# Kernel tuning notes

Measured on AMD Instinct MI355X. Metric: run time of the kernel, lower is better.

## Reference

```python
import jax, jax.numpy as jnp
import numpy as np

B = 16384
D = 384
K = 256
BETAS = (0.05, 0.25, 0.6)  # per-level commitment costs


def setup_inputs() -> dict:
    key = jax.random.key(0)
    k0, k1, k2, kc0, kc1, kc2 = jax.random.split(key, 6)
    return {
        "l0": jax.random.normal(k0, (B, 4, D), dtype=jnp.float32),
        "l1": jax.random.normal(k1, (B, 16, D), dtype=jnp.float32),
        "l2": jax.random.normal(k2, (B, 16, D), dtype=jnp.float32),
        "cb0": jax.random.normal(kc0, (K, D), dtype=jnp.float32),
        "cb1": jax.random.normal(kc1, (K, D), dtype=jnp.float32),
        "cb2": jax.random.normal(kc2, (K, D), dtype=jnp.float32),
    }


def _vq(x, cb, beta):
    # x: (B, T, D), cb: (K, D) -> d2: (B, T, K)
    d2 = (jnp.sum(x * x, axis=-1, keepdims=True)
          - 2.0 * jnp.einsum('btd,kd->btk', x, cb)
          + jnp.sum(cb * cb, axis=-1))
    idx = jnp.argmin(d2, axis=-1)            # (B, T) nearest codebook entry
    q = cb[idx]                              # (B, T, D) gather
    # EMA-VQ: codebook updated by EMA, loss is commitment term only
    loss = beta * jnp.mean((jax.lax.stop_gradient(q) - x) ** 2)
    q_st = x + jax.lax.stop_gradient(q - x)  # straight-through estimator
    return q_st, loss, idx


def reference(l0, l1, l2, cb0, cb1, cb2):
    q0, loss0, idx0 = _vq(l0, cb0, BETAS[0])
    q1, loss1, idx1 = _vq(l1, cb1, BETAS[1])
    q2, loss2, idx2 = _vq(l2, cb2, BETAS[2])
    total_vq_loss = loss0 + loss1 + loss2
    return (q0, q1, q2, total_vq_loss, idx0, idx1, idx2)
```

## Files before the change

kernel.cpp:

```cpp
#include <hip/hip_runtime.h>

static constexpr int KN  = 256;
static constexpr int DD  = 384;
static constexpr int DD4 = 96;
static constexpr int TM  = 64;
#define FLAG_MARGIN 0.005f

typedef __attribute__((ext_vector_type(8)))  short bf16x8;
typedef __attribute__((ext_vector_type(16))) float f32x16;
typedef __attribute__((ext_vector_type(4)))  short short4v;

__device__ __forceinline__ unsigned short f2bf_rne(float x) {
  unsigned u = __float_as_uint(x);
  return (unsigned short)((u + 0x7fffu + ((u >> 16) & 1u)) >> 16);
}

__device__ __forceinline__ void g2lds16(const void* g, void* l) {
  __builtin_amdgcn_global_load_lds(
      (const __attribute__((address_space(1))) unsigned int*)g,
      (__attribute__((address_space(3))) unsigned int*)l, 16, 0, 0);
}

__device__ __forceinline__ float emu_sq_pairwise384(const float* __restrict__ p) {
  float S[4];
#pragma unroll
  for (int blk = 0; blk < 4; ++blk) {
    const float* b = p + blk * 96;
    float r[8];
#pragma unroll
    for (int l = 0; l < 8; ++l) r[l] = __fmul_rn(b[l], b[l]);
    for (int j = 8; j < 96; j += 8) {
#pragma unroll
      for (int l = 0; l < 8; ++l) r[l] = __fadd_rn(r[l], __fmul_rn(b[j + l], b[j + l]));
    }
    float t1 = __fadd_rn(__fadd_rn(r[0], r[1]), __fadd_rn(r[2], r[3]));
    float t2 = __fadd_rn(__fadd_rn(r[4], r[5]), __fadd_rn(r[6], r[7]));
    S[blk] = __fadd_rn(t1, t2);
  }
  return __fadd_rn(__fadd_rn(S[0], S[1]), __fadd_rn(S[2], S[3]));
}

__device__ __forceinline__ float emu_dot384_np(const float* __restrict__ x,
                                               const float* __restrict__ c) {
  float s[16];
#pragma unroll
  for (int t = 0; t < 16; ++t) s[t] = 0.f;
  for (int j = 0; j < 384; j += 16) {
#pragma unroll
    for (int t = 0; t < 16; ++t)
      s[t] = __fadd_rn(__fmul_rn(x[j + t], c[j + t]), s[t]);
  }
  float w0 = __fadd_rn(__fadd_rn(s[0], s[4]), __fadd_rn(s[8],  s[12]));
  float w1 = __fadd_rn(__fadd_rn(s[1], s[5]), __fadd_rn(s[9],  s[13]));
  float w2 = __fadd_rn(__fadd_rn(s[2], s[6]), __fadd_rn(s[10], s[14]));
  float w3 = __fadd_rn(__fadd_rn(s[3], s[7]), __fadd_rn(s[11], s[15]));
  return __fadd_rn(__fadd_rn(w0, w1), __fadd_rn(w2, w3));
}

__global__ __launch_bounds__(256) void prep_kernel(const float* __restrict__ c0,
                                                   const float* __restrict__ c1,
                                                   const float* __restrict__ c2,
                                                   float* __restrict__ e2,
                                                   double* __restrict__ delta,
                                                   short* __restrict__ fragbase) {
  int bid = blockIdx.x;
  if (bid < 3) {
    const float* cb = (bid == 0) ? c0 : ((bid == 1) ? c1 : c2);
    e2[bid * KN + threadIdx.x] = emu_sq_pairwise384(cb + (size_t)threadIdx.x * DD);
    if (threadIdx.x == 0) delta[bid] = 0.0;
    return;
  }
  int sb = bid - 3;
  int lvl = sb / 48;
  int blk48 = sb - lvl * 48;
  const float* cb = (lvl == 0) ? c0 : ((lvl == 1) ? c1 : c2);
  short* frag = fragbase + (size_t)lvl * 196608;
  int gid = blk48 * 256 + threadIdx.x;
  int e = gid / 48;
  int g = gid - e * 48;
  const float4* s4 = reinterpret_cast<const float4*>(cb) + (size_t)e * 96 + g * 2;
  float4 v0 = s4[0], v1 = s4[1];
  float xs[8] = {v0.x, v0.y, v0.z, v0.w, v1.x, v1.y, v1.z, v1.w};
  short h[8], l[8];
#pragma unroll
  for (int i = 0; i < 8; ++i) {
    h[i] = (short)f2bf_rne(xs[i]);
    float hf = __uint_as_float((unsigned)(unsigned short)h[i] << 16);
    l[i] = (short)f2bf_rne(xs[i] - hf);
  }
  int c = g >> 2, rem = g & 3, ks = rem >> 1, hs = rem & 1;
  int t = e >> 5, lane = (e & 31) + (hs << 5);
  size_t blk = (((size_t)(c * 8 + t) * 2 + ks) * 2);
  short* dh = frag + blk * 512 + lane * 8;
  short* dl = dh + 512;
  *reinterpret_cast<bf16x8*>(dh) = *reinterpret_cast<const bf16x8*>(h);
  *reinterpret_cast<bf16x8*>(dl) = *reinterpret_cast<const bf16x8*>(l);
}

__global__ __launch_bounds__(512) void vq_main(
    const float* __restrict__ X0, const float* __restrict__ X1, const float* __restrict__ X2,
    const float* __restrict__ C0, const float* __restrict__ C1, const float* __restrict__ C2,
    const short* __restrict__ FRAGBASE,
    const float* __restrict__ E2A,
    float* __restrict__ QBASE,
    float* __restrict__ IDXBASE,
    unsigned char* __restrict__ FLAGBASE,
    double* __restrict__ PART,
    int nb0, int nb1)
{
  __shared__ __align__(16) short cb_lds[16384];
  __shared__ __align__(16) short x_lds[4096];
  struct Epi {
    float b1[8][TM]; int i1[8][TM]; float b2[8][TM];
    int idx[TM]; float xx[TM];
  };
  Epi* ep = reinterpret_cast<Epi*>(x_lds);

  const int bid = blockIdx.x;
  int lvl, lb;
  if (bid < nb0)            { lvl = 0; lb = bid; }
  else if (bid < nb0 + nb1) { lvl = 1; lb = bid - nb0; }
  else                      { lvl = 2; lb = bid - nb0 - nb1; }
  const float* X  = (lvl == 0) ? X0 : ((lvl == 1) ? X1 : X2);
  const float* CBF32 = (lvl == 0) ? C0 : ((lvl == 1) ? C1 : C2);
  const short* CBFRAG = FRAGBASE + (size_t)lvl * 196608;
  const float* E2 = E2A + lvl * KN;
  const size_t rowbase = (lvl == 0) ? 0 : ((lvl == 1) ? (size_t)nb0 * TM
                                                      : (size_t)(nb0 + nb1) * TM);
  float* Q = QBASE + rowbase * DD;
  float* IDXO = IDXBASE + rowbase;
  unsigned char* FLAG = FLAGBASE + rowbase;
  const size_t row0 = (size_t)lb * TM;

  const int tid  = threadIdx.x;
  const int wid  = tid >> 6, lane = tid & 63;
  const int lr   = lane & 31, hi = lane >> 5;
  const int r_st = tid >> 3, k4 = tid & 7;

  const float4* X4 = reinterpret_cast<const float4*>(X);
  const float4* xsrc = X4 + (row0 + (size_t)r_st) * DD4 + k4;

  f32x16 acc[2];
  {
    f32x16 z;
#pragma unroll
    for (int i = 0; i < 16; ++i) z[i] = 0.f;
    acc[0] = z; acc[1] = z;
  }
  float xx = 0.f;

  const int xblk = ((r_st >> 5) * 2 + (k4 >> 2)) * 2;
  const int xpos = (((k4 >> 1) & 1) * 32 + (r_st & 31)) * 16 + (k4 & 1) * 8;

#pragma unroll 1
  for (int c = 0; c < 12; ++c) {
#pragma unroll
    for (int s = 0; s < 4; ++s) {
      int idx = s * 512 + tid;
      int b = idx >> 6;
      const char* src = (const char*)CBFRAG
          + (((size_t)(c * 8 + (b >> 2)) * 4 + (b & 3)) << 10) + (idx & 63) * 16;
      g2lds16(src, (char*)cb_lds + idx * 16);
    }
    {
      float4 v = xsrc[c * 8];
      float a_[4] = {v.x, v.y, v.z, v.w};
      short hh_[4], ll_[4];
#pragma unroll
      for (int i = 0; i < 4; ++i) {
        xx = fmaf(a_[i], a_[i], xx);
        unsigned u_ = __float_as_uint(a_[i]);
        unsigned t_ = u_ + 0x7fffu + ((u_ >> 16) & 1u);
        hh_[i] = (short)(t_ >> 16);
        float hf_ = __uint_as_float(t_ & 0xffff0000u);
        float lf_ = a_[i] - hf_;
        ll_[i] = (short)(__float_as_uint(lf_) >> 16);
      }
      char* xb_ = (char*)x_lds;
      *reinterpret_cast<short4v*>(xb_ + xblk * 1024 + xpos) =
          *reinterpret_cast<short4v*>(hh_);
      *reinterpret_cast<short4v*>(xb_ + (xblk + 1) * 1024 + xpos) =
          *reinterpret_cast<short4v*>(ll_);
    }
    __syncthreads();

    const char* xb = (const char*)x_lds;
    const char* bbase = (const char*)cb_lds;
#pragma unroll
    for (int ks = 0; ks < 2; ++ks) {
      bf16x8 ah0 = *reinterpret_cast<const bf16x8*>(xb + ((0 * 2 + ks) * 2 + 0) * 1024 + lane * 16);
      bf16x8 al0 = *reinterpret_cast<const bf16x8*>(xb + ((0 * 2 + ks) * 2 + 1) * 1024 + lane * 16);
      bf16x8 ah1 = *reinterpret_cast<const bf16x8*>(xb + ((1 * 2 + ks) * 2 + 0) * 1024 + lane * 16);
      bf16x8 al1 = *reinterpret_cast<const bf16x8*>(xb + ((1 * 2 + ks) * 2 + 1) * 1024 + lane * 16);
      bf16x8 bh = *reinterpret_cast<const bf16x8*>(bbase + (wid * 4 + ks * 2 + 0) * 1024 + lane * 16);
      bf16x8 bl = *reinterpret_cast<const bf16x8*>(bbase + (wid * 4 + ks * 2 + 1) * 1024 + lane * 16);
      acc[0] = __builtin_amdgcn_mfma_f32_32x32x16_bf16(ah0, bh, acc[0], 0, 0, 0);
      acc[0] = __builtin_amdgcn_mfma_f32_32x32x16_bf16(ah0, bl, acc[0], 0, 0, 0);
      acc[0] = __builtin_amdgcn_mfma_f32_32x32x16_bf16(al0, bh, acc[0], 0, 0, 0);
      acc[1] = __builtin_amdgcn_mfma_f32_32x32x16_bf16(ah1, bh, acc[1], 0, 0, 0);
      acc[1] = __builtin_amdgcn_mfma_f32_32x32x16_bf16(ah1, bl, acc[1], 0, 0, 0);
      acc[1] = __builtin_amdgcn_mfma_f32_32x32x16_bf16(al1, bh, acc[1], 0, 0, 0);
    }
    __syncthreads();
  }

  {
    float t = xx;
    t += __shfl_xor(t, 1);
    t += __shfl_xor(t, 2);
    t += __shfl_xor(t, 4);
    if ((lane & 7) == 0) ep->xx[r_st] = t;
  }

  const float e2v = E2[wid * 32 + lr];
  const int mycol = wid * 32 + lr;

#pragma unroll
  for (int rt = 0; rt < 2; ++rt) {
#pragma unroll
    for (int v = 0; v < 16; ++v) {
      int row = rt * 32 + (v & 3) + 8 * (v >> 2) + 4 * hi;
      float sc = e2v - 2.0f * acc[rt][v];
      float b1 = sc; int i1 = mycol;
#pragma unroll
      for (int m = 1; m < 32; m <<= 1) {
        float ob = __shfl_xor(b1, m);
        int   oi = __shfl_xor(i1, m);
        if (ob < b1 || (ob == b1 && oi < i1)) { b1 = ob; i1 = oi; }
      }
      float b2 = (mycol != i1) ? sc : 1e30f;
#pragma unroll
      for (int m = 1; m < 32; m <<= 1) {
        float ob = __shfl_xor(b2, m);
        if (ob < b2) b2 = ob;
      }
      if (lr == 0) {
        ep->b1[wid][row] = b1; ep->i1[wid][row] = i1; ep->b2[wid][row] = b2;
      }
    }
  }
  __syncthreads();

  double lrow = 0.0;
  if (tid < TM) {
    float b1 = ep->b1[0][tid]; int i1 = ep->i1[0][tid]; float b2 = ep->b2[0][tid];
#pragma unroll
    for (int w = 1; w < 8; ++w) {
      float ob1 = ep->b1[w][tid]; int oi1 = ep->i1[w][tid]; float ob2 = ep->b2[w][tid];
      if (ob1 < b1 || (ob1 == b1 && oi1 < i1)) {
        b2 = fminf(b1, ob2); b1 = ob1; i1 = oi1;
      } else {
        b2 = fminf(b2, ob1);
      }
    }
    ep->idx[tid] = i1;
    IDXO[row0 + tid] = (float)i1;
    FLAG[row0 + tid] = (b2 - b1 < FLAG_MARGIN) ? 1 : 0;
    lrow = (double)ep->xx[tid] + (double)b1;
  }
  if (tid < 64) {
#pragma unroll
    for (int m = 1; m < 64; m <<= 1) lrow += __shfl_xor(lrow, m);
    if (tid == 0) PART[bid] = lrow;
  }
  __syncthreads();

  const float4* CB4 = reinterpret_cast<const float4*>(CBF32);
  float4* Q4 = reinterpret_cast<float4*>(Q);
  for (int i = tid; i < TM * DD4; i += 512) {
    int r = i / DD4;
    int cc = i - r * DD4;
    Q4[(row0 + (size_t)r) * DD4 + cc] = CB4[(size_t)ep->idx[r] * DD4 + cc];
  }
}

__global__ __launch_bounds__(256) void vq_refine(
    const float* __restrict__ X0, const float* __restrict__ X1, const float* __restrict__ X2,
    const float* __restrict__ C0, const float* __restrict__ C1, const float* __restrict__ C2,
    const float* __restrict__ E2A,
    const unsigned char* __restrict__ F0, const unsigned char* __restrict__ F1,
    const unsigned char* __restrict__ F2,
    int r0, int r1, int r2,
    float* __restrict__ Q0, float* __restrict__ Q1, float* __restrict__ Q2,
    float* __restrict__ I0, float* __restrict__ I1, float* __restrict__ I2,
    double* __restrict__ DELTA)
{
  const int lane   = threadIdx.x & 63;
  const int gwave  = (blockIdx.x * blockDim.x + threadIdx.x) >> 6;
  const int nwaves = (gridDim.x * blockDim.x) >> 6;
  const int ntot = r0 + r1 + r2;

  for (int base = gwave * 64; base < ntot; base += nwaves * 64) {
    int lvl, lb;
    const float *X, *CB; const unsigned char* FLAG; float *Q, *IDXO;
    if (base < r0)           { lvl = 0; lb = base;            X = X0; CB = C0; FLAG = F0; Q = Q0; IDXO = I0; }
    else if (base < r0 + r1) { lvl = 1; lb = base - r0;       X = X1; CB = C1; FLAG = F1; Q = Q1; IDXO = I1; }
    else                     { lvl = 2; lb = base - r0 - r1;  X = X2; CB = C2; FLAG = F2; Q = Q2; IDXO = I2; }
    const float* E2EMU = E2A + lvl * KN;

    unsigned char f = FLAG[lb + lane];
    unsigned long long mask = __ballot(f != 0);
    while (mask) {
      int bit = __ffsll((long long)mask) - 1;
      mask &= mask - 1;
      const int r = lb + bit;
      const float* xr = X + (size_t)r * DD;
      const float xx = emu_sq_pairwise384(xr);

      float best = 1e30f; int bidx = 0x7fffffff;
#pragma unroll
      for (int t = 0; t < 4; ++t) {
        int k = lane * 4 + t;
        const float* ck = CB + (size_t)k * DD;
        float E = emu_dot384_np(xr, ck);
        float s = __fadd_rn(__fsub_rn(xx, __fmul_rn(2.0f, E)), E2EMU[k]);
        if (s < best || (s == best && k < bidx)) { best = s; bidx = k; }
      }
#pragma unroll
      for (int m = 1; m < 64; m <<= 1) {
        float ob = __shfl_xor(best, m);
        int   oi = __shfl_xor(bidx, m);
        if (ob < best || (ob == best && oi < bidx)) { best = ob; bidx = oi; }
      }

      const int old = (int)IDXO[r];
      if (bidx != old) {
        const float* cn = CB + (size_t)bidx * DD;
        const float* co = CB + (size_t)old * DD;
        double dl = 0.0;
        for (int d = lane; d < DD; d += 64) {
          float xv = xr[d];
          float qn = cn[d], qo = co[d];
          Q[(size_t)r * DD + d] = qn;
          double en = (double)qn - (double)xv;
          double eo = (double)qo - (double)xv;
          dl += en * en - eo * eo;
        }
#pragma unroll
        for (int m = 1; m < 64; m <<= 1) dl += __shfl_xor(dl, m);
        if (lane == 0) {
          atomicAdd(DELTA + lvl, dl);
          IDXO[r] = (float)bidx;
        }
      }
    }
  }
}

__global__ void finalize_kernel(const double* __restrict__ p0, int n0, double w0,
                                const double* __restrict__ p1, int n1, double w1,
                                const double* __restrict__ p2, int n2, double w2,
                                const double* __restrict__ delta,
                                float* __restrict__ out) {
  __shared__ double red[4];
  int tid = threadIdx.x;
  double s0 = 0.0, s1 = 0.0, s2 = 0.0;
  for (int i = tid; i < n0; i += 256) s0 += p0[i];
  for (int i = tid; i < n1; i += 256) s1 += p1[i];
  for (int i = tid; i < n2; i += 256) s2 += p2[i];
  double v = s0 * w0 + s1 * w1 + s2 * w2;
#pragma unroll
  for (int m = 1; m < 64; m <<= 1) v += __shfl_xor(v, m);
  if ((tid & 63) == 0) red[tid >> 6] = v;
  __syncthreads();
  if (tid == 0)
    out[0] = (float)(red[0] + red[1] + red[2] + red[3]
                     + delta[0] * w0 + delta[1] * w1 + delta[2] * w2);
}

extern "C" void kernel_launch(void* const* d_in, const int* in_sizes, int n_in,
                              void* d_out, int out_size, void* d_ws, size_t ws_size,
                              hipStream_t stream) {
  const float* l0  = (const float*)d_in[0];
  const float* l1  = (const float*)d_in[1];
  const float* l2  = (const float*)d_in[2];
  const float* cb0 = (const float*)d_in[3];
  const float* cb1 = (const float*)d_in[4];
  const float* cb2 = (const float*)d_in[5];

  const size_t n_q0 = (size_t)in_sizes[0];
  const size_t n_q1 = (size_t)in_sizes[1];
  const size_t n_q2 = (size_t)in_sizes[2];
  const int r0 = (int)(n_q0 / DD);
  const int r1 = (int)(n_q1 / DD);
  const int r2 = (int)(n_q2 / DD);

  float* out   = (float*)d_out;
  float* q0    = out;
  float* q1    = q0 + n_q0;
  float* q2    = q1 + n_q1;
  float* lossp = q2 + n_q2;
  float* idx0  = lossp + 1;
  float* idx1  = idx0 + r0;
  float* idx2  = idx1 + r1;

  float*  e2    = (float*)d_ws;
  double* part  = (double*)((char*)d_ws + 4096);
  double* delta = (double*)((char*)d_ws + 4096 + 73728);
  unsigned char* flag0 = (unsigned char*)d_ws + 4096 + 73728 + 1024;
  unsigned char* flag1 = flag0 + r0;
  unsigned char* flag2 = flag1 + r1;
  short* cbf0 = (short*)((char*)d_ws + (1 << 20));

  const int nb0 = r0 / TM, nb1 = r1 / TM, nb2 = r2 / TM;
  double* p0 = part;
  double* p1 = p0 + nb0;
  double* p2 = p1 + nb1;

  prep_kernel<<<147, 256, 0, stream>>>(cb0, cb1, cb2, e2, delta, cbf0);

  vq_main<<<nb0 + nb1 + nb2, 512, 0, stream>>>(
      l0, l1, l2, cb0, cb1, cb2, cbf0, e2,
      q0, idx0, flag0, part, nb0, nb1);

  vq_refine<<<512, 256, 0, stream>>>(l0, l1, l2, cb0, cb1, cb2, e2,
                                     flag0, flag1, flag2, r0, r1, r2,
                                     q0, q1, q2, idx0, idx1, idx2, delta);

  const double w0 = 0.05 / ((double)r0 * DD);
  const double w1 = 0.25 / ((double)r1 * DD);
  const double w2 = 0.60 / ((double)r2 * DD);
  finalize_kernel<<<1, 256, 0, stream>>>(p0, nb0, w0, p1, nb1, w1, p2, nb2, w2,
                                         delta, lossp);
}
```

Baseline: 898.0 us.

## Double-buffer codebook and x tiles in LDS to overlap loads with MFMA

Splits the K-loop into 24 half-size chunks and keeps two LDS buffers for the codebook fragments and the converted x tile. The next chunk's global-to-LDS copy and x conversion are issued while MFMAs run on the current buffer, leaving one barrier per chunk. The aim is to hide global load latency behind matrix math, at the cost of more barriers overall and smaller work per phase. The epilogue scratch now aliases the codebook buffer instead of the x buffer.

```diff
diff --git a/kernel.cpp b/kernel.cpp
--- a/kernel.cpp
+++ b/kernel.cpp
@@ -8,7 +8,6 @@
 
 typedef __attribute__((ext_vector_type(8)))  short bf16x8;
 typedef __attribute__((ext_vector_type(16))) float f32x16;
-typedef __attribute__((ext_vector_type(4)))  short short4v;
 
 __device__ __forceinline__ unsigned short f2bf_rne(float x) {
   unsigned u = __float_as_uint(x);
@@ -108,13 +107,13 @@
     double* __restrict__ PART,
     int nb0, int nb1)
 {
-  __shared__ __align__(16) short cb_lds[16384];
-  __shared__ __align__(16) short x_lds[4096];
+  __shared__ __align__(16) short cb_lds[2][8192];
+  __shared__ __align__(16) short x_lds[2][2048];
   struct Epi {
     float b1[8][TM]; int i1[8][TM]; float b2[8][TM];
     int idx[TM]; float xx[TM];
   };
-  Epi* ep = reinterpret_cast<Epi*>(x_lds);
+  Epi* ep = reinterpret_cast<Epi*>(&cb_lds[0][0]);
 
   const int bid = blockIdx.x;
   int lvl, lb;
@@ -135,10 +134,10 @@
   const int tid  = threadIdx.x;
   const int wid  = tid >> 6, lane = tid & 63;
   const int lr   = lane & 31, hi = lane >> 5;
-  const int r_st = tid >> 3, k4 = tid & 7;
-
-  const float4* X4 = reinterpret_cast<const float4*>(X);
-  const float4* xsrc = X4 + (row0 + (size_t)r_st) * DD4 + k4;
+  const int r_st = tid >> 3, k2 = tid & 7;
+
+  const float2* xsrc2 = reinterpret_cast<const float2*>(X)
+                        + (row0 + (size_t)r_st) * 192 + k2;
 
   f32x16 acc[2];
   {
@@ -149,57 +148,83 @@
   }
   float xx = 0.f;
 
-  const int xblk = ((r_st >> 5) * 2 + (k4 >> 2)) * 2;
-  const int xpos = (((k4 >> 1) & 1) * 32 + (r_st & 31)) * 16 + (k4 & 1) * 8;
+  const int xblk2 = (r_st >> 5) * 2;
+  const int xpos  = (((k2 >> 2) * 32 + (r_st & 31)) * 16) + (k2 & 3) * 4;
+
+#define STAGE_CB(CN)                                                          \
+  {                                                                           \
+    const int par_ = (CN) & 1;                                                \
+    _Pragma("unroll")                                                         \
+    for (int s = 0; s < 2; ++s) {                                             \
+      int idx = s * 512 + tid;                                   \
+      int b = idx >> 6;                            \
+      const char* src = (const char*)CBFRAG                                   \
+          + ((((size_t)((CN) >> 1) * 8 + (b >> 1)) * 4 + ((CN) & 1) * 2       \
+              + (b & 1)) << 10) + (idx & 63) * 16;                            \
+      g2lds16(src, (char*)cb_lds[par_] + idx * 16);                           \
+    }                                                                         \
+  }
+
+#define CVT_WRITE_X(CN, XF)                                                   \
+  {                                                                           \
+    float a0_ = (XF).x, a1_ = (XF).y;                                         \
+    xx = fmaf(a0_, a0_, xx); xx = fmaf(a1_, a1_, xx);                         \
+    unsigned u0_ = __float_as_uint(a0_);                                      \
+    unsigned t0_ = u0_ + 0x7fffu + ((u0_ >> 16) & 1u);                        \
+    unsigned u1_ = __float_as_uint(a1_);                                      \
+    unsigned t1_ = u1_ + 0x7fffu + ((u1_ >> 16) & 1u);                        \
+    unsigned hp_ = (t0_ >> 16) | (t1_ & 0xffff0000u);                         \
+    float l0_ = a0_ - __uint_as_float(t0_ & 0xffff0000u);                     \
+    float l1_ = a1_ - __uint_as_float(t1_ & 0xffff0000u);                     \
+    unsigned lp_ = (__float_as_uint(l0_) >> 16)                               \
+                   | (__float_as_uint(l1_) & 0xffff0000u);                    \
+    char* xb_ = (char*)x_lds[(CN) & 1];                                       \
+    *reinterpret_cast<unsigned*>(xb_ + xblk2 * 1024 + xpos)        = hp_;     \
+    *reinterpret_cast<unsigned*>(xb_ + (xblk2 + 1) * 1024 + xpos)  = lp_;     \
+  }
+
+#define MFMA_PHASE(CN)                                                        \
+  {                                                                           \
+    const char* xb_ = (const char*)x_lds[(CN) & 1];                           \
+    bf16x8 ah0 = *reinterpret_cast<const bf16x8*>(xb_ +        lane * 16);    \
+    bf16x8 al0 = *reinterpret_cast<const bf16x8*>(xb_ + 1024 + lane * 16);    \
+    bf16x8 ah1 = *reinterpret_cast<const bf16x8*>(xb_ + 2048 + lane * 16);    \
+    bf16x8 al1 = *reinterpret_cast<const bf16x8*>(xb_ + 3072 + lane * 16);    \
+    const char* bb_ = (const char*)cb_lds[(CN) & 1];                          \
+    bf16x8 bh = *reinterpret_cast<const bf16x8*>(bb_ + (wid * 2 + 0) * 1024   \
+                                                 + lane * 16);                \
+    bf16x8 bl = *reinterpret_cast<const bf16x8*>(bb_ + (wid * 2 + 1) * 1024   \
+                                                 + lane * 16);                \
+    acc[0] = __builtin_amdgcn_mfma_f32_32x32x16_bf16(ah0, bh, acc[0], 0, 0, 0);\
+    acc[0] = __builtin_amdgcn_mfma_f32_32x32x16_bf16(ah0, bl, acc[0], 0, 0, 0);\
+    acc[0] = __builtin_amdgcn_mfma_f32_32x32x16_bf16(al0, bh, acc[0], 0, 0, 0);\
+    acc[1] = __builtin_amdgcn_mfma_f32_32x32x16_bf16(ah1, bh, acc[1], 0, 0, 0);\
+    acc[1] = __builtin_amdgcn_mfma_f32_32x32x16_bf16(ah1, bl, acc[1], 0, 0, 0);\
+    acc[1] = __builtin_amdgcn_mfma_f32_32x32x16_bf16(al1, bh, acc[1], 0, 0, 0);\
+  }
+
+  float2 xfA = xsrc2[0];
+  float2 xfB;
+  STAGE_CB(0);
+  CVT_WRITE_X(0, xfA);
+  xfA = xsrc2[8];
+  __syncthreads();
 
 #pragma unroll 1
-  for (int c = 0; c < 12; ++c) {
-#pragma unroll
-    for (int s = 0; s < 4; ++s) {
-      int idx = s * 512 + tid;
-      int b = idx >> 6;
-      const char* src = (const char*)CBFRAG
-          + (((size_t)(c * 8 + (b >> 2)) * 4 + (b & 3)) << 10) + (idx & 63) * 16;
-      g2lds16(src, (char*)cb_lds + idx * 16);
-    }
-    {
-      float4 v = xsrc[c * 8];
-      float a_[4] = {v.x, v.y, v.z, v.w};
-      short hh_[4], ll_[4];
-#pragma unroll
-      for (int i = 0; i < 4; ++i) {
-        xx = fmaf(a_[i], a_[i], xx);
-        unsigned u_ = __float_as_uint(a_[i]);
-        unsigned t_ = u_ + 0x7fffu + ((u_ >> 16) & 1u);
-        hh_[i] = (short)(t_ >> 16);
-        float hf_ = __uint_as_float(t_ & 0xffff0000u);
-        float lf_ = a_[i] - hf_;
-        ll_[i] = (short)(__float_as_uint(lf_) >> 16);
-      }
-      char* xb_ = (char*)x_lds;
-      *reinterpret_cast<short4v*>(xb_ + xblk * 1024 + xpos) =
-          *reinterpret_cast<short4v*>(hh_);
-      *reinterpret_cast<short4v*>(xb_ + (xblk + 1) * 1024 + xpos) =
-          *reinterpret_cast<short4v*>(ll_);
-    }
+  for (int cc = 0; cc < 12; ++cc) {
+    const int c0 = 2 * cc, c1 = 2 * cc + 1;
+    STAGE_CB(c0 + 1);
+    if (c0 < 22) xfB = xsrc2[(c0 + 2) * 8];
+    MFMA_PHASE(c0);
+    CVT_WRITE_X(c0 + 1, xfA);
     __syncthreads();
-
-    const char* xb = (const char*)x_lds;
-    const char* bbase = (const char*)cb_lds;
-#pragma unroll
-    for (int ks = 0; ks < 2; ++ks) {
-      bf16x8 ah0 = *reinterpret_cast<const bf16x8*>(xb + ((0 * 2 + ks) * 2 + 0) * 1024 + lane * 16);
-      bf16x8 al0 = *reinterpret_cast<const bf16x8*>(xb + ((0 * 2 + ks) * 2 + 1) * 1024 + lane * 16);
-      bf16x8 ah1 = *reinterpret_cast<const bf16x8*>(xb + ((1 * 2 + ks) * 2 + 0) * 1024 + lane * 16);
-      bf16x8 al1 = *reinterpret_cast<const bf16x8*>(xb + ((1 * 2 + ks) * 2 + 1) * 1024 + lane * 16);
-      bf16x8 bh = *reinterpret_cast<const bf16x8*>(bbase + (wid * 4 + ks * 2 + 0) * 1024 + lane * 16);
-      bf16x8 bl = *reinterpret_cast<const bf16x8*>(bbase + (wid * 4 + ks * 2 + 1) * 1024 + lane * 16);
-      acc[0] = __builtin_amdgcn_mfma_f32_32x32x16_bf16(ah0, bh, acc[0], 0, 0, 0);
-      acc[0] = __builtin_amdgcn_mfma_f32_32x32x16_bf16(ah0, bl, acc[0], 0, 0, 0);
-      acc[0] = __builtin_amdgcn_mfma_f32_32x32x16_bf16(al0, bh, acc[0], 0, 0, 0);
-      acc[1] = __builtin_amdgcn_mfma_f32_32x32x16_bf16(ah1, bh, acc[1], 0, 0, 0);
-      acc[1] = __builtin_amdgcn_mfma_f32_32x32x16_bf16(ah1, bl, acc[1], 0, 0, 0);
-      acc[1] = __builtin_amdgcn_mfma_f32_32x32x16_bf16(al1, bh, acc[1], 0, 0, 0);
+    if (c1 < 23) {
+      STAGE_CB(c1 + 1);
+      if (c1 < 22) xfA = xsrc2[(c1 + 2) * 8];
+      MFMA_PHASE(c1);
+      CVT_WRITE_X(c1 + 1, xfB);
+    } else {
+      MFMA_PHASE(23);
     }
     __syncthreads();
   }
@@ -209,7 +234,7 @@
     t += __shfl_xor(t, 1);
     t += __shfl_xor(t, 2);
     t += __shfl_xor(t, 4);
-    if ((lane & 7) == 0) ep->xx[r_st] = t;
+    if ((tid & 7) == 0) ep->xx[r_st] = t;
   }
 
   const float e2v = E2[wid * 32 + lr];
```

Measured after the change: 1.093 ms. 1.22x slower.
